# Optimization experiments

Measured on AMD Instinct MI355X. Metric: run time of the kernel, lower is better.

The kernel has to match this reference:

```python
import jax, jax.numpy as jnp
import numpy as np

NUM_LOOP = 10


def gru_cell(x, h, W_ih, W_hh, b_ih, b_hh):
    # torch.nn.GRUCell math. x, h: [N, H]; W_ih, W_hh: [3H, H]; b: [3H]
    gi = x @ W_ih.T + b_ih
    gh = h @ W_hh.T + b_hh
    i_r, i_z, i_n = jnp.split(gi, 3, axis=-1)
    h_r, h_z, h_n = jnp.split(gh, 3, axis=-1)
    r = jax.nn.sigmoid(i_r + h_r)
    z = jax.nn.sigmoid(i_z + h_z)
    n = jnp.tanh(i_n + r * h_n)
    return (1.0 - z) * n + z * h


def setup_inputs() -> dict:
    key = jax.random.key(0)
    ks = jax.random.split(key, 16)
    B, S, L, H, V = 16, 128, 128, 128, 50000
    input_var = jax.random.randint(ks[0], (B, S, L), 0, V, dtype=jnp.int32)
    adjacency = (jax.random.uniform(ks[1], (B, S, L, L)) < 0.05).astype(jnp.float32)
    u = lambda k, shp, a: jax.random.uniform(k, shp, minval=-a, maxval=a, dtype=jnp.float32)
    emb = jax.random.normal(ks[2], (V, H), dtype=jnp.float32) * 0.1
    gnn_w = u(ks[3], (H, H), 0.08)
    gnn_b = u(ks[4], (H,), 0.08)
    W_ih = u(ks[5], (3 * H, H), 0.08)
    W_hh = u(ks[6], (3 * H, H), 0.08)
    b_ih = u(ks[7], (3 * H,), 0.08)
    b_hh = u(ks[8], (3 * H,), 0.08)
    mW1 = u(ks[9], (H, H), 0.08)
    mb1 = u(ks[10], (H,), 0.08)
    mW2 = u(ks[11], (H, H), 0.08)
    mb2 = u(ks[12], (H,), 0.08)
    mW3 = u(ks[13], (1, H), 0.08)
    mb3 = u(ks[14], (1,), 0.08)
    return dict(input_var=input_var, adjacency=adjacency, emb=emb, gnn_w=gnn_w,
                gnn_b=gnn_b, W_ih=W_ih, W_hh=W_hh, b_ih=b_ih, b_hh=b_hh,
                mW1=mW1, mb1=mb1, mW2=mW2, mb2=mb2, mW3=mW3, mb3=mb3)


def reference(input_var, adjacency, emb, gnn_w, gnn_b, W_ih, W_hh, b_ih, b_hh,
              mW1, mb1, mW2, mb2, mW3, mb3):
    B, S, L = input_var.shape
    H = emb.shape[1]
    node_feature = emb[input_var]  # [B, S, L, H]

    def body(i, nf):
        tmp = nf @ gnn_w + gnn_b                      # [B,S,L,H] linear transform
        agg = jnp.matmul(adjacency, tmp)              # [B,S,L,L] @ [B,S,L,H]
        h = gru_cell(agg.reshape(-1, H), nf.reshape(-1, H), W_ih, W_hh, b_ih, b_hh)
        return h.reshape(B, S, L, H)

    node_feature = jax.lax.fori_loop(0, NUM_LOOP, body, node_feature)
    x = node_feature.reshape(B, S * L, H)
    # mention_predictor: 3-layer MLP with tanh after every layer (incl. last)
    h1 = jnp.tanh(x @ mW1.T + mb1)
    h2 = jnp.tanh(h1 @ mW2.T + mb2)
    mention_score = jnp.tanh(h2 @ mW3.T + mb3)        # [B, S*L, 1]
    return mention_score.reshape(B, S * L)
```

## Files before the change

kernel.cpp:

```cpp
#include <hip/hip_runtime.h>
#include <stdint.h>

typedef __bf16 bf16x8 __attribute__((ext_vector_type(8)));
typedef float  f32x4  __attribute__((ext_vector_type(4)));
typedef unsigned short ushortx4 __attribute__((ext_vector_type(4)));

#define LDS_NFROW 0
#define LDS_NFT   32768
#define LDS_P     65536
#define LDS_SAT   98304
#define LDS_RSA   131072
#define LDS_GB2   131584
#define LDS_BIH   133120
#define LDS_BHH   134656
#define LDS_MB1   136192
#define LDS_MB2   136704
#define LDS_TOTAL 137216

#define WS_GW2T   0
#define WS_WHH    98304
#define WS_MW1    196608
#define WS_MW2    229376
#define WS_GB2    262144

__device__ __forceinline__ unsigned short f2bf(float f){
  union{float f; uint32_t u;} v; v.f = f;
  return (unsigned short)((v.u + 0x7FFFu + ((v.u>>16)&1u)) >> 16);
}
__device__ __forceinline__ float bf2f(unsigned short h){
  union{uint32_t u; float f;} v; v.u = ((uint32_t)h)<<16; return v.f;
}
__device__ __forceinline__ float fast_sigmoid(float x){
  float t = __builtin_amdgcn_exp2f(-1.442695041f*x);
  return __builtin_amdgcn_rcpf(1.0f + t);
}
__device__ __forceinline__ float fast_tanh(float x){
  float t = __builtin_amdgcn_exp2f(-2.885390082f*x);
  return 2.0f*__builtin_amdgcn_rcpf(1.0f + t) - 1.0f;
}
__device__ __forceinline__ uint32_t sw(uint32_t row, uint32_t col){
  return row*256u + ((((col>>3) ^ (row&7)) << 4) | ((col&7)<<1));
}

extern "C" __global__ __launch_bounds__(128) void gnn_prep(
    const float* __restrict__ Wih, const float* __restrict__ Whh,
    const float* __restrict__ gnnw, const float* __restrict__ gnnb,
    const float* __restrict__ mW1, const float* __restrict__ mW2,
    unsigned short* __restrict__ gw2t, unsigned short* __restrict__ whhb,
    unsigned short* __restrict__ mw1b, unsigned short* __restrict__ mw2b,
    float* __restrict__ gb2)
{
  __shared__ float wg[128];
  const int b = blockIdx.x, t = threadIdx.x;
  if (b < 384){
    wg[t] = Wih[b*128 + t];
    __syncthreads();
    float acc = 0.f;
    for (int h=0; h<128; ++h) acc += wg[h] * gnnw[t*128 + h];
    gw2t[b*128 + t] = f2bf(acc);
    if (t == 0){
      float a2 = 0.f;
      for (int h=0; h<128; ++h) a2 += wg[h] * gnnb[h];
      gb2[b] = a2;
    }
  } else if (b < 416){
    int base = (b-384)*1536;
    for (int i=t; i<1536; i+=128) whhb[base+i] = f2bf(Whh[base+i]);
  } else if (b < 432){
    int base = (b-416)*1024;
    for (int i=t; i<1024; i+=128) mw1b[base+i] = f2bf(mW1[base+i]);
  } else if (b < 448){
    int base = (b-432)*1024;
    for (int i=t; i<1024; i+=128) mw2b[base+i] = f2bf(mW2[base+i]);
  }
}

extern "C" __global__ __launch_bounds__(512) void gnn_main(
    const int* __restrict__ iv, const float* __restrict__ adj,
    const float* __restrict__ emb,
    const float* __restrict__ bih, const float* __restrict__ bhh,
    const float* __restrict__ mb1, const float* __restrict__ mb2,
    const float* __restrict__ mW3, const float* __restrict__ mb3,
    const __bf16* __restrict__ gw2t, const __bf16* __restrict__ whhb,
    const __bf16* __restrict__ mw1b, const __bf16* __restrict__ mw2b,
    const float* __restrict__ gb2, float* __restrict__ out)
{
  extern __shared__ char lds[];
  const int bs   = blockIdx.x;
  const int tid  = threadIdx.x;
  const int w    = tid >> 6;
  const int lane = tid & 63;
  const int n16  = lane & 15;
  const int q    = lane >> 4;
  const f32x4 zf4 = {0.f, 0.f, 0.f, 0.f};

  if (tid < 384){
    *(float*)(lds + LDS_GB2 + tid*4) = gb2[tid];
    *(float*)(lds + LDS_BIH + tid*4) = bih[tid];
    *(float*)(lds + LDS_BHH + tid*4) = bhh[tid];
  }
  if (tid >= 384){
    int t = tid - 384;
    *(float*)(lds + LDS_MB1 + t*4) = mb1[t];
    *(float*)(lds + LDS_MB2 + t*4) = mb2[t];
  }

  {
    const int l  = tid >> 2;
    const int hc = (tid & 3) * 32;
    const int row = iv[bs*128 + l];
    const float* src = emb + (size_t)row*128 + hc;
    #pragma unroll
    for (int c=0; c<4; ++c){
      float4 f0 = *(const float4*)(src + c*8);
      float4 f1 = *(const float4*)(src + c*8 + 4);
      union{ bf16x8 v; unsigned short s8[8]; } u;
      u.s8[0]=f2bf(f0.x); u.s8[1]=f2bf(f0.y); u.s8[2]=f2bf(f0.z); u.s8[3]=f2bf(f0.w);
      u.s8[4]=f2bf(f1.x); u.s8[5]=f2bf(f1.y); u.s8[6]=f2bf(f1.z); u.s8[7]=f2bf(f1.w);
      *(bf16x8*)(lds + LDS_NFROW + sw(l, hc + c*8)) = u.v;
      #pragma unroll
      for (int j=0; j<8; ++j)
        *(unsigned short*)(lds + LDS_NFT + sw(hc + c*8 + j, l)) = u.s8[j];
    }
  }

  {
    const float* abase = adj + (size_t)bs * 16384;
    #pragma unroll
    for (int k=0; k<4; ++k){
      int s   = k*512 + tid;
      int sl  = s & 63;
      int chk = s >> 6;
      int ltg = chk >> 2, ks = chk & 3;
      int al  = ltg*16 + (sl & 15);
      int ak  = ks*32 + (sl >> 4) * 8;
      const float* p = abase + al*128 + ak;
      float4 f0 = *(const float4*)(p);
      float4 f1 = *(const float4*)(p + 4);
      union{ bf16x8 v; unsigned short s8[8]; } u;
      u.s8[0]=f2bf(f0.x); u.s8[1]=f2bf(f0.y); u.s8[2]=f2bf(f0.z); u.s8[3]=f2bf(f0.w);
      u.s8[4]=f2bf(f1.x); u.s8[5]=f2bf(f1.y); u.s8[6]=f2bf(f1.z); u.s8[7]=f2bf(f1.w);
      *(bf16x8*)(lds + LDS_SAT + s*16) = u.v;
    }
    int l = tid >> 2, p4 = tid & 3;
    const float* p = abase + l*128 + p4*32;
    float ssum = 0.f;
    #pragma unroll
    for (int c=0; c<8; ++c){
      float4 f = *(const float4*)(p + c*4);
      ssum += f.x + f.y + f.z + f.w;
    }
    ssum += __shfl_xor(ssum, 1);
    ssum += __shfl_xor(ssum, 2);
    if (p4 == 0) *(float*)(lds + LDS_RSA + l*4) = ssum;
  }
  __syncthreads();

  const int wr = w & 1, wc = w >> 1;
  const int t0 = wr*64, l0 = wc*32;
  const int h0 = w*16;

  const __bf16* gAr = gw2t + (size_t)(h0       + n16) * 128;
  const __bf16* gAz = gw2t + (size_t)(h0 + 128 + n16) * 128;
  const __bf16* gAn = gw2t + (size_t)(h0 + 256 + n16) * 128;
  const __bf16* hAr = whhb + (size_t)(h0       + n16) * 128;
  const __bf16* hAz = whhb + (size_t)(h0 + 128 + n16) * 128;
  const __bf16* hAn = whhb + (size_t)(h0 + 256 + n16) * 128;

  for (int it=0; it<10; ++it){
    f32x4 accA[4][2];
    #pragma unroll
    for (int a=0; a<4; ++a){ accA[a][0] = zf4; accA[a][1] = zf4; }
    for (int ks=0; ks<4; ++ks){
      bf16x8 af[4];
      #pragma unroll
      for (int tt=0; tt<4; ++tt)
        af[tt] = *(const bf16x8*)(lds + LDS_NFT + sw(t0 + tt*16 + n16, ks*32 + q*8));
      #pragma unroll
      for (int lb=0; lb<2; ++lb){
        int chunk = (wc*2 + lb)*4 + ks;
        bf16x8 bfb = *(const bf16x8*)(lds + LDS_SAT + (chunk*64 + lane)*16);
        #pragma unroll
        for (int tt=0; tt<4; ++tt)
          accA[tt][lb] = __builtin_amdgcn_mfma_f32_16x16x32_bf16(af[tt], bfb, accA[tt][lb], 0,0,0);
      }
    }
    #pragma unroll
    for (int tt=0; tt<4; ++tt){
      #pragma unroll
      for (int lb=0; lb<2; ++lb){
        int l  = l0 + lb*16 + n16;
        int tb = t0 + tt*16 + q*4;
        ushortx4 o4;
        #pragma unroll
        for (int r=0; r<4; ++r) o4[r] = f2bf(accA[tt][lb][r]);
        *(ushortx4*)(lds + LDS_P + sw(l, tb)) = o4;
      }
    }
    __syncthreads();

    f32x4 aR[8], aZ[8], aGN[8], aHN[8];
    #pragma unroll
    for (int i=0; i<8; ++i){ aR[i]=zf4; aZ[i]=zf4; aGN[i]=zf4; aHN[i]=zf4; }
    for (int ks=0; ks<4; ++ks){
      int koff = ks*32 + q*8;
      bf16x8 f_gr = *(const bf16x8*)(gAr + koff);
      bf16x8 f_gz = *(const bf16x8*)(gAz + koff);
      bf16x8 f_gn = *(const bf16x8*)(gAn + koff);
      bf16x8 f_hr = *(const bf16x8*)(hAr + koff);
      bf16x8 f_hz = *(const bf16x8*)(hAz + koff);
      bf16x8 f_hn = *(const bf16x8*)(hAn + koff);
      #pragma unroll
      for (int lt=0; lt<8; ++lt){
        int l = lt*16 + n16;
        bf16x8 bp = *(const bf16x8*)(lds + LDS_P     + sw(l, koff));
        bf16x8 bh = *(const bf16x8*)(lds + LDS_NFROW + sw(l, koff));
        aR[lt]  = __builtin_amdgcn_mfma_f32_16x16x32_bf16(f_gr, bp, aR[lt], 0,0,0);
        aR[lt]  = __builtin_amdgcn_mfma_f32_16x16x32_bf16(f_hr, bh, aR[lt], 0,0,0);
        aZ[lt]  = __builtin_amdgcn_mfma_f32_16x16x32_bf16(f_gz, bp, aZ[lt], 0,0,0);
        aZ[lt]  = __builtin_amdgcn_mfma_f32_16x16x32_bf16(f_hz, bh, aZ[lt], 0,0,0);
        aGN[lt] = __builtin_amdgcn_mfma_f32_16x16x32_bf16(f_gn, bp, aGN[lt], 0,0,0);
        aHN[lt] = __builtin_amdgcn_mfma_f32_16x16x32_bf16(f_hn, bh, aHN[lt], 0,0,0);
      }
    }
    __syncthreads();

    float c_gr[4], c_gz[4], c_gn[4], c_br[4], c_bz[4], c_bin[4], c_bhn[4];
    #pragma unroll
    for (int r=0; r<4; ++r){
      int h = h0 + q*4 + r;
      c_gr[r]  = *(const float*)(lds + LDS_GB2 + h*4);
      c_gz[r]  = *(const float*)(lds + LDS_GB2 + (128+h)*4);
      c_gn[r]  = *(const float*)(lds + LDS_GB2 + (256+h)*4);
      c_br[r]  = *(const float*)(lds + LDS_BIH + h*4)       + *(const float*)(lds + LDS_BHH + h*4);
      c_bz[r]  = *(const float*)(lds + LDS_BIH + (128+h)*4) + *(const float*)(lds + LDS_BHH + (128+h)*4);
      c_bin[r] = *(const float*)(lds + LDS_BIH + (256+h)*4);
      c_bhn[r] = *(const float*)(lds + LDS_BHH + (256+h)*4);
    }
    #pragma unroll
    for (int lt=0; lt<8; ++lt){
      int l = lt*16 + n16;
      float rs = *(const float*)(lds + LDS_RSA + l*4);
      uint32_t a_nf = sw(l, h0 + q*4);
      ushortx4 old4 = *(const ushortx4*)(lds + LDS_NFROW + a_nf);
      ushortx4 new4;
      #pragma unroll
      for (int r=0; r<4; ++r){
        float xr = aR[lt][r] + rs*c_gr[r] + c_br[r];
        float xz = aZ[lt][r] + rs*c_gz[r] + c_bz[r];
        float rg = fast_sigmoid(xr);
        float zg = fast_sigmoid(xz);
        float xn = (aGN[lt][r] + rs*c_gn[r] + c_bin[r]) + rg*(aHN[lt][r] + c_bhn[r]);
        float ng = fast_tanh(xn);
        float hv = bf2f(old4[r]);
        new4[r] = f2bf(ng + zg*(hv - ng));
      }
      *(ushortx4*)(lds + LDS_NFROW + a_nf) = new4;
      #pragma unroll
      for (int r=0; r<4; ++r)
        *(unsigned short*)(lds + LDS_NFT + sw(h0 + q*4 + r, l)) = new4[r];
    }
    __syncthreads();
  }

  {
    f32x4 acc[4][2];
    #pragma unroll
    for (int a=0; a<4; ++a){ acc[a][0] = zf4; acc[a][1] = zf4; }
    for (int ks=0; ks<4; ++ks){
      int koff = ks*32 + q*8;
      bf16x8 af[4];
      #pragma unroll
      for (int tt=0; tt<4; ++tt)
        af[tt] = *(const bf16x8*)(mw1b + (size_t)(t0 + tt*16 + n16)*128 + koff);
      #pragma unroll
      for (int lb=0; lb<2; ++lb){
        int l = l0 + lb*16 + n16;
        bf16x8 bb = *(const bf16x8*)(lds + LDS_NFROW + sw(l, koff));
        #pragma unroll
        for (int tt=0; tt<4; ++tt)
          acc[tt][lb] = __builtin_amdgcn_mfma_f32_16x16x32_bf16(af[tt], bb, acc[tt][lb], 0,0,0);
      }
    }
    #pragma unroll
    for (int tt=0; tt<4; ++tt){
      #pragma unroll
      for (int lb=0; lb<2; ++lb){
        int l  = l0 + lb*16 + n16;
        int ob = t0 + tt*16 + q*4;
        ushortx4 o4;
        #pragma unroll
        for (int r=0; r<4; ++r){
          float bsv = *(const float*)(lds + LDS_MB1 + (ob + r)*4);
          o4[r] = f2bf(fast_tanh(acc[tt][lb][r] + bsv));
        }
        *(ushortx4*)(lds + LDS_P + sw(l, ob)) = o4;
      }
    }
  }
  __syncthreads();

  {
    f32x4 acc[4][2];
    #pragma unroll
    for (int a=0; a<4; ++a){ acc[a][0] = zf4; acc[a][1] = zf4; }
    for (int ks=0; ks<4; ++ks){
      int koff = ks*32 + q*8;
      bf16x8 af[4];
      #pragma unroll
      for (int tt=0; tt<4; ++tt)
        af[tt] = *(const bf16x8*)(mw2b + (size_t)(t0 + tt*16 + n16)*128 + koff);
      #pragma unroll
      for (int lb=0; lb<2; ++lb){
        int l = l0 + lb*16 + n16;
        bf16x8 bb = *(const bf16x8*)(lds + LDS_P + sw(l, koff));
        #pragma unroll
        for (int tt=0; tt<4; ++tt)
          acc[tt][lb] = __builtin_amdgcn_mfma_f32_16x16x32_bf16(af[tt], bb, acc[tt][lb], 0,0,0);
      }
    }
    #pragma unroll
    for (int tt=0; tt<4; ++tt){
      #pragma unroll
      for (int lb=0; lb<2; ++lb){
        int l  = l0 + lb*16 + n16;
        int ob = t0 + tt*16 + q*4;
        ushortx4 o4;
        #pragma unroll
        for (int r=0; r<4; ++r){
          float bsv = *(const float*)(lds + LDS_MB2 + (ob + r)*4);
          o4[r] = f2bf(fast_tanh(acc[tt][lb][r] + bsv));
        }
        *(ushortx4*)(lds + LDS_NFT + sw(l, ob)) = o4;
      }
    }
  }
  __syncthreads();

  {
    int l = tid >> 2, p4 = tid & 3;
    float dot = 0.f;
    #pragma unroll
    for (int c=0; c<4; ++c){
      int o = p4*32 + c*8;
      union{ bf16x8 v; unsigned short s8[8]; } u;
      u.v = *(const bf16x8*)(lds + LDS_NFT + sw(l, o));
      float4 w0 = *(const float4*)(mW3 + o);
      float4 w1 = *(const float4*)(mW3 + o + 4);
      dot += bf2f(u.s8[0])*w0.x + bf2f(u.s8[1])*w0.y + bf2f(u.s8[2])*w0.z + bf2f(u.s8[3])*w0.w
           + bf2f(u.s8[4])*w1.x + bf2f(u.s8[5])*w1.y + bf2f(u.s8[6])*w1.z + bf2f(u.s8[7])*w1.w;
    }
    dot += __shfl_xor(dot, 1);
    dot += __shfl_xor(dot, 2);
    if (p4 == 0) out[bs*128 + l] = fast_tanh(dot + mb3[0]);
  }
}

extern "C" void kernel_launch(void* const* d_in, const int* in_sizes, int n_in,
                              void* d_out, int out_size, void* d_ws, size_t ws_size,
                              hipStream_t stream)
{
  const int*   iv   = (const int*)  d_in[0];
  const float* adj  = (const float*)d_in[1];
  const float* emb  = (const float*)d_in[2];
  const float* gnnw = (const float*)d_in[3];
  const float* gnnb = (const float*)d_in[4];
  const float* Wih  = (const float*)d_in[5];
  const float* Whh  = (const float*)d_in[6];
  const float* bihp = (const float*)d_in[7];
  const float* bhhp = (const float*)d_in[8];
  const float* mW1  = (const float*)d_in[9];
  const float* mb1  = (const float*)d_in[10];
  const float* mW2  = (const float*)d_in[11];
  const float* mb2  = (const float*)d_in[12];
  const float* mW3  = (const float*)d_in[13];
  const float* mb3  = (const float*)d_in[14];
  float* out = (float*)d_out;

  char* ws = (char*)d_ws;
  unsigned short* gw2t_w = (unsigned short*)(ws + WS_GW2T);
  unsigned short* whhb_w = (unsigned short*)(ws + WS_WHH);
  unsigned short* mw1b_w = (unsigned short*)(ws + WS_MW1);
  unsigned short* mw2b_w = (unsigned short*)(ws + WS_MW2);
  float*          gb2_w  = (float*)(ws + WS_GB2);

  hipFuncSetAttribute((const void*)gnn_main,
                      hipFuncAttributeMaxDynamicSharedMemorySize, LDS_TOTAL);

  gnn_prep<<<448, 128, 0, stream>>>(Wih, Whh, gnnw, gnnb, mW1, mW2,
                                    gw2t_w, whhb_w, mw1b_w, mw2b_w, gb2_w);

  int nbs = in_sizes[0] / 128;
  gnn_main<<<nbs, 512, LDS_TOTAL, stream>>>(
      iv, adj, emb, bihp, bhhp, mb1, mb2, mW3, mb3,
      (const __bf16*)gw2t_w, (const __bf16*)whhb_w,
      (const __bf16*)mw1b_w, (const __bf16*)mw2b_w, gb2_w, out);
}
```

Before: 2.244 ms.

## Double block to 1024 threads and stream adjacency from global each iteration

Doubles the workgroup to 16 waves and re-splits every GEMM stage across them: each wave now owns 16 hidden rows by 64 columns in the GNN loop and 32x32 tiles in the MLP. The bf16 adjacency copy in LDS is removed, and adjacency is reloaded from global (fp32, converted each iteration) inside the aggregation loop. This cuts LDS use and register pressure per wave so more waves can hide latency. The biases are packed into one per-row structure and the swizzle gets an extra XOR term to reduce bank conflicts. The cost is ten re-reads of the adjacency tile from global or cache plus repeated conversion work.

```diff
diff --git a/kernel.cpp b/kernel.cpp
--- a/kernel.cpp
+++ b/kernel.cpp
@@ -8,14 +8,11 @@
 #define LDS_NFROW 0
 #define LDS_NFT   32768
 #define LDS_P     65536
-#define LDS_SAT   98304
-#define LDS_RSA   131072
-#define LDS_GB2   131584
-#define LDS_BIH   133120
-#define LDS_BHH   134656
-#define LDS_MB1   136192
-#define LDS_MB2   136704
-#define LDS_TOTAL 137216
+#define LDS_RSA   98304
+#define LDS_CB    98816
+#define LDS_MB1   102912
+#define LDS_MB2   103424
+#define LDS_TOTAL 103936
 
 #define WS_GW2T   0
 #define WS_WHH    98304
@@ -39,7 +36,7 @@
   return 2.0f*__builtin_amdgcn_rcpf(1.0f + t) - 1.0f;
 }
 __device__ __forceinline__ uint32_t sw(uint32_t row, uint32_t col){
-  return row*256u + ((((col>>3) ^ (row&7)) << 4) | ((col&7)<<1));
+  return row*256u + ((((col>>3) ^ (row&7) ^ ((row>>3)&3)) << 4) | ((col&7)<<1));
 }
 
 extern "C" __global__ __launch_bounds__(128) void gnn_prep(
@@ -75,7 +72,7 @@
   }
 }
 
-extern "C" __global__ __launch_bounds__(512) void gnn_main(
+extern "C" __global__ __launch_bounds__(1024) void gnn_main(
     const int* __restrict__ iv, const float* __restrict__ adj,
     const float* __restrict__ emb,
     const float* __restrict__ bih, const float* __restrict__ bhh,
@@ -94,163 +91,141 @@
   const int q    = lane >> 4;
   const f32x4 zf4 = {0.f, 0.f, 0.f, 0.f};
 
-  if (tid < 384){
-    *(float*)(lds + LDS_GB2 + tid*4) = gb2[tid];
-    *(float*)(lds + LDS_BIH + tid*4) = bih[tid];
-    *(float*)(lds + LDS_BHH + tid*4) = bhh[tid];
-  }
-  if (tid >= 384){
-    int t = tid - 384;
+  const int hw = w >> 1, lc = w & 1;
+  const int t0  = hw*16;
+  const int h0  = t0;
+  const int lG0 = lc*64;
+  const int wr = w >> 2, wc = w & 3;
+  const int tm0 = wr*32, lm0 = wc*32;
+
+  if (tid < 128){
+    int h = tid;
+    float* cb = (float*)(lds + LDS_CB + h*32);
+    cb[0] = gb2[h]; cb[1] = gb2[128+h]; cb[2] = gb2[256+h];
+    cb[3] = bih[h] + bhh[h];
+    cb[4] = bih[128+h] + bhh[128+h];
+    cb[5] = bih[256+h];
+    cb[6] = bhh[256+h];
+    cb[7] = 0.f;
+  } else if (tid < 256){
+    int t = tid - 128;
     *(float*)(lds + LDS_MB1 + t*4) = mb1[t];
     *(float*)(lds + LDS_MB2 + t*4) = mb2[t];
   }
-
   {
-    const int l  = tid >> 2;
-    const int hc = (tid & 3) * 32;
+    const int l   = tid >> 3;
+    const int hc8 = (tid & 7) * 16;
     const int row = iv[bs*128 + l];
-    const float* src = emb + (size_t)row*128 + hc;
-    #pragma unroll
-    for (int c=0; c<4; ++c){
+    const float* src = emb + (size_t)row*128 + hc8;
+    #pragma unroll
+    for (int c=0; c<2; ++c){
       float4 f0 = *(const float4*)(src + c*8);
       float4 f1 = *(const float4*)(src + c*8 + 4);
       union{ bf16x8 v; unsigned short s8[8]; } u;
       u.s8[0]=f2bf(f0.x); u.s8[1]=f2bf(f0.y); u.s8[2]=f2bf(f0.z); u.s8[3]=f2bf(f0.w);
       u.s8[4]=f2bf(f1.x); u.s8[5]=f2bf(f1.y); u.s8[6]=f2bf(f1.z); u.s8[7]=f2bf(f1.w);
-      *(bf16x8*)(lds + LDS_NFROW + sw(l, hc + c*8)) = u.v;
+      *(bf16x8*)(lds + LDS_NFROW + sw(l, hc8 + c*8)) = u.v;
       #pragma unroll
       for (int j=0; j<8; ++j)
-        *(unsigned short*)(lds + LDS_NFT + sw(hc + c*8 + j, l)) = u.s8[j];
-    }
-  }
-
-  {
-    const float* abase = adj + (size_t)bs * 16384;
-    #pragma unroll
-    for (int k=0; k<4; ++k){
-      int s   = k*512 + tid;
-      int sl  = s & 63;
-      int chk = s >> 6;
-      int ltg = chk >> 2, ks = chk & 3;
-      int al  = ltg*16 + (sl & 15);
-      int ak  = ks*32 + (sl >> 4) * 8;
-      const float* p = abase + al*128 + ak;
-      float4 f0 = *(const float4*)(p);
-      float4 f1 = *(const float4*)(p + 4);
-      union{ bf16x8 v; unsigned short s8[8]; } u;
-      u.s8[0]=f2bf(f0.x); u.s8[1]=f2bf(f0.y); u.s8[2]=f2bf(f0.z); u.s8[3]=f2bf(f0.w);
-      u.s8[4]=f2bf(f1.x); u.s8[5]=f2bf(f1.y); u.s8[6]=f2bf(f1.z); u.s8[7]=f2bf(f1.w);
-      *(bf16x8*)(lds + LDS_SAT + s*16) = u.v;
-    }
-    int l = tid >> 2, p4 = tid & 3;
-    const float* p = abase + l*128 + p4*32;
-    float ssum = 0.f;
-    #pragma unroll
-    for (int c=0; c<8; ++c){
-      float4 f = *(const float4*)(p + c*4);
-      ssum += f.x + f.y + f.z + f.w;
-    }
-    ssum += __shfl_xor(ssum, 1);
-    ssum += __shfl_xor(ssum, 2);
-    if (p4 == 0) *(float*)(lds + LDS_RSA + l*4) = ssum;
+        *(unsigned short*)(lds + LDS_NFT + sw(hc8 + c*8 + j, l)) = u.s8[j];
+    }
+    const float* ap = adj + (size_t)bs*16384 + l*128 + hc8;
+    float s = 0.f;
+    #pragma unroll
+    for (int c=0; c<4; ++c){
+      float4 f = *(const float4*)(ap + c*4);
+      s += f.x + f.y + f.z + f.w;
+    }
+    s += __shfl_xor(s, 1);
+    s += __shfl_xor(s, 2);
+    s += __shfl_xor(s, 4);
+    if ((tid & 7) == 0) *(float*)(lds + LDS_RSA + l*4) = s;
   }
   __syncthreads();
 
-  const int wr = w & 1, wc = w >> 1;
-  const int t0 = wr*64, l0 = wc*32;
-  const int h0 = w*16;
-
-  const __bf16* gAr = gw2t + (size_t)(h0       + n16) * 128;
-  const __bf16* gAz = gw2t + (size_t)(h0 + 128 + n16) * 128;
-  const __bf16* gAn = gw2t + (size_t)(h0 + 256 + n16) * 128;
-  const __bf16* hAr = whhb + (size_t)(h0       + n16) * 128;
-  const __bf16* hAz = whhb + (size_t)(h0 + 128 + n16) * 128;
-  const __bf16* hAn = whhb + (size_t)(h0 + 256 + n16) * 128;
+  const __bf16* gR = gw2t + (size_t)(h0       + n16) * 128;
+  const __bf16* gZ = gw2t + (size_t)(h0 + 128 + n16) * 128;
+  const __bf16* gN = gw2t + (size_t)(h0 + 256 + n16) * 128;
+  const __bf16* hR = whhb + (size_t)(h0       + n16) * 128;
+  const __bf16* hZ = whhb + (size_t)(h0 + 128 + n16) * 128;
+  const __bf16* hN = whhb + (size_t)(h0 + 256 + n16) * 128;
+  const float*  abase = adj + (size_t)bs * 16384;
 
   for (int it=0; it<10; ++it){
-    f32x4 accA[4][2];
-    #pragma unroll
-    for (int a=0; a<4; ++a){ accA[a][0] = zf4; accA[a][1] = zf4; }
+    f32x4 accA[4];
+    #pragma unroll
+    for (int j=0; j<4; ++j) accA[j] = zf4;
     for (int ks=0; ks<4; ++ks){
-      bf16x8 af[4];
-      #pragma unroll
-      for (int tt=0; tt<4; ++tt)
-        af[tt] = *(const bf16x8*)(lds + LDS_NFT + sw(t0 + tt*16 + n16, ks*32 + q*8));
-      #pragma unroll
-      for (int lb=0; lb<2; ++lb){
-        int chunk = (wc*2 + lb)*4 + ks;
-        bf16x8 bfb = *(const bf16x8*)(lds + LDS_SAT + (chunk*64 + lane)*16);
-        #pragma unroll
-        for (int tt=0; tt<4; ++tt)
-          accA[tt][lb] = __builtin_amdgcn_mfma_f32_16x16x32_bf16(af[tt], bfb, accA[tt][lb], 0,0,0);
-      }
-    }
-    #pragma unroll
-    for (int tt=0; tt<4; ++tt){
-      #pragma unroll
-      for (int lb=0; lb<2; ++lb){
-        int l  = l0 + lb*16 + n16;
-        int tb = t0 + tt*16 + q*4;
-        ushortx4 o4;
-        #pragma unroll
-        for (int r=0; r<4; ++r) o4[r] = f2bf(accA[tt][lb][r]);
-        *(ushortx4*)(lds + LDS_P + sw(l, tb)) = o4;
-      }
-    }
-    __syncthreads();
-
-    f32x4 aR[8], aZ[8], aGN[8], aHN[8];
-    #pragma unroll
-    for (int i=0; i<8; ++i){ aR[i]=zf4; aZ[i]=zf4; aGN[i]=zf4; aHN[i]=zf4; }
+      bf16x8 af = *(const bf16x8*)(lds + LDS_NFT + sw(t0 + n16, ks*32 + q*8));
+      #pragma unroll
+      for (int j=0; j<4; ++j){
+        int al = lG0 + j*16 + n16;
+        const float* ap = abase + al*128 + ks*32 + q*8;
+        float4 a0 = *(const float4*)(ap);
+        float4 a1 = *(const float4*)(ap + 4);
+        union{ bf16x8 v; unsigned short s8[8]; } u;
+        u.s8[0]=f2bf(a0.x); u.s8[1]=f2bf(a0.y); u.s8[2]=f2bf(a0.z); u.s8[3]=f2bf(a0.w);
+        u.s8[4]=f2bf(a1.x); u.s8[5]=f2bf(a1.y); u.s8[6]=f2bf(a1.z); u.s8[7]=f2bf(a1.w);
+        accA[j] = __builtin_amdgcn_mfma_f32_16x16x32_bf16(af, u.v, accA[j], 0,0,0);
+      }
+    }
+    #pragma unroll
+    for (int j=0; j<4; ++j){
+      int l = lG0 + j*16 + n16;
+      ushortx4 o4;
+      #pragma unroll
+      for (int r=0; r<4; ++r) o4[r] = f2bf(accA[j][r]);
+      *(ushortx4*)(lds + LDS_P + sw(l, t0 + q*4)) = o4;
+    }
+    __syncthreads();
+
+    f32x4 aR[4], aZ[4], aGN[4], aHN[4];
+    #pragma unroll
+    for (int i=0; i<4; ++i){ aR[i]=zf4; aZ[i]=zf4; aGN[i]=zf4; aHN[i]=zf4; }
     for (int ks=0; ks<4; ++ks){
       int koff = ks*32 + q*8;
-      bf16x8 f_gr = *(const bf16x8*)(gAr + koff);
-      bf16x8 f_gz = *(const bf16x8*)(gAz + koff);
-      bf16x8 f_gn = *(const bf16x8*)(gAn + koff);
-      bf16x8 f_hr = *(const bf16x8*)(hAr + koff);
-      bf16x8 f_hz = *(const bf16x8*)(hAz + koff);
-      bf16x8 f_hn = *(const bf16x8*)(hAn + koff);
-      #pragma unroll
-      for (int lt=0; lt<8; ++lt){
-        int l = lt*16 + n16;
+      bf16x8 f_gr = *(const bf16x8*)(gR + koff);
+      bf16x8 f_gz = *(const bf16x8*)(gZ + koff);
+      bf16x8 f_gn = *(const bf16x8*)(gN + koff);
+      bf16x8 f_hr = *(const bf16x8*)(hR + koff);
+      bf16x8 f_hz = *(const bf16x8*)(hZ + koff);
+      bf16x8 f_hn = *(const bf16x8*)(hN + koff);
+      #pragma unroll
+      for (int lt=0; lt<4; ++lt){
+        int l = lG0 + lt*16 + n16;
         bf16x8 bp = *(const bf16x8*)(lds + LDS_P     + sw(l, koff));
         bf16x8 bh = *(const bf16x8*)(lds + LDS_NFROW + sw(l, koff));
         aR[lt]  = __builtin_amdgcn_mfma_f32_16x16x32_bf16(f_gr, bp, aR[lt], 0,0,0);
+        aZ[lt]  = __builtin_amdgcn_mfma_f32_16x16x32_bf16(f_gz, bp, aZ[lt], 0,0,0);
+        aGN[lt] = __builtin_amdgcn_mfma_f32_16x16x32_bf16(f_gn, bp, aGN[lt], 0,0,0);
         aR[lt]  = __builtin_amdgcn_mfma_f32_16x16x32_bf16(f_hr, bh, aR[lt], 0,0,0);
-        aZ[lt]  = __builtin_amdgcn_mfma_f32_16x16x32_bf16(f_gz, bp, aZ[lt], 0,0,0);
         aZ[lt]  = __builtin_amdgcn_mfma_f32_16x16x32_bf16(f_hz, bh, aZ[lt], 0,0,0);
-        aGN[lt] = __builtin_amdgcn_mfma_f32_16x16x32_bf16(f_gn, bp, aGN[lt], 0,0,0);
         aHN[lt] = __builtin_amdgcn_mfma_f32_16x16x32_bf16(f_hn, bh, aHN[lt], 0,0,0);
       }
     }
     __syncthreads();
 
-    float c_gr[4], c_gz[4], c_gn[4], c_br[4], c_bz[4], c_bin[4], c_bhn[4];
+    f32x4 cbA[4], cbB[4];
     #pragma unroll
     for (int r=0; r<4; ++r){
       int h = h0 + q*4 + r;
-      c_gr[r]  = *(const float*)(lds + LDS_GB2 + h*4);
-      c_gz[r]  = *(const float*)(lds + LDS_GB2 + (128+h)*4);
-      c_gn[r]  = *(const float*)(lds + LDS_GB2 + (256+h)*4);
-      c_br[r]  = *(const float*)(lds + LDS_BIH + h*4)       + *(const float*)(lds + LDS_BHH + h*4);
-      c_bz[r]  = *(const float*)(lds + LDS_BIH + (128+h)*4) + *(const float*)(lds + LDS_BHH + (128+h)*4);
-      c_bin[r] = *(const float*)(lds + LDS_BIH + (256+h)*4);
-      c_bhn[r] = *(const float*)(lds + LDS_BHH + (256+h)*4);
-    }
-    #pragma unroll
-    for (int lt=0; lt<8; ++lt){
-      int l = lt*16 + n16;
+      cbA[r] = *(const f32x4*)(lds + LDS_CB + h*32);
+      cbB[r] = *(const f32x4*)(lds + LDS_CB + h*32 + 16);
+    }
+    #pragma unroll
+    for (int lt=0; lt<4; ++lt){
+      int l = lG0 + lt*16 + n16;
       float rs = *(const float*)(lds + LDS_RSA + l*4);
       uint32_t a_nf = sw(l, h0 + q*4);
       ushortx4 old4 = *(const ushortx4*)(lds + LDS_NFROW + a_nf);
       ushortx4 new4;
       #pragma unroll
       for (int r=0; r<4; ++r){
-        float xr = aR[lt][r] + rs*c_gr[r] + c_br[r];
-        float xz = aZ[lt][r] + rs*c_gz[r] + c_bz[r];
+        float xr = aR[lt][r] + rs*cbA[r][0] + cbA[r][3];
+        float xz = aZ[lt][r] + rs*cbA[r][1] + cbB[r][0];
         float rg = fast_sigmoid(xr);
         float zg = fast_sigmoid(xz);
-        float xn = (aGN[lt][r] + rs*c_gn[r] + c_bin[r]) + rg*(aHN[lt][r] + c_bhn[r]);
+        float xn = (aGN[lt][r] + rs*cbA[r][2] + cbB[r][1]) + rg*(aHN[lt][r] + cbB[r][2]);
         float ng = fast_tanh(xn);
         float hv = bf2f(old4[r]);
         new4[r] = f2bf(ng + zg*(hv - ng));
@@ -264,30 +239,31 @@
   }
 
   {
-    f32x4 acc[4][2];
-    #pragma unroll
-    for (int a=0; a<4; ++a){ acc[a][0] = zf4; acc[a][1] = zf4; }
+    f32x4 acc[2][2];
+    #pragma unroll
+    for (int a=0; a<2; ++a){ acc[a][0] = zf4; acc[a][1] = zf4; }
     for (int ks=0; ks<4; ++ks){
       int koff = ks*32 + q*8;
-      bf16x8 af[4];
-      #pragma unroll
-      for (int tt=0; tt<4; ++tt)
-        af[tt] = *(const bf16x8*)(mw1b + (size_t)(t0 + tt*16 + n16)*128 + koff);
+      bf16x8 af[2];
+      #pragma unroll
+      for (int tt=0; tt<2; ++tt)
+        af[tt] = *(const bf16x8*)(mw1b + (size_t)(tm0 + tt*16 + n16)*128 + koff);
       #pragma unroll
       for (int lb=0; lb<2; ++lb){
-        int l = l0 + lb*16 + n16;
+        int l = lm0 + lb*16 + n16;
         bf16x8 bb = *(const bf16x8*)(lds + LDS_NFROW + sw(l, koff));
         #pragma unroll
-        for (int tt=0; tt<4; ++tt)
+        for (int tt=0; tt<2; ++tt)
           acc[tt][lb] = __builtin_amdgcn_mfma_f32_16x16x32_bf16(af[tt], bb, acc[tt][lb], 0,0,0);
       }
     }
-    #pragma unroll
-    for (int tt=0; tt<4; ++tt){
+    __syncthreads();
+    #pragma unroll
+    for (int tt=0; tt<2; ++tt){
       #pragma unroll
       for (int lb=0; lb<2; ++lb){
-        int l  = l0 + lb*16 + n16;
-        int ob = t0 + tt*16 + q*4;
+        int l  = lm0 + lb*16 + n16;
+        int ob = tm0 + tt*16 + q*4;
         ushortx4 o4;
         #pragma unroll
         for (int r=0; r<4; ++r){
@@ -301,30 +277,30 @@
   __syncthreads();
 
   {
-    f32x4 acc[4][2];
-    #pragma unroll
-    for (int a=0; a<4; ++a){ acc[a][0] = zf4; acc[a][1] = zf4; }
+    f32x4 acc[2][2];
+    #pragma unroll
+    for (int a=0; a<2; ++a){ acc[a][0] = zf4; acc[a][1] = zf4; }
     for (int ks=0; ks<4; ++ks){
       int koff = ks*32 + q*8;
-      bf16x8 af[4];
-      #pragma unroll
-      for (int tt=0; tt<4; ++tt)
-        af[tt] = *(const bf16x8*)(mw2b + (size_t)(t0 + tt*16 + n16)*128 + koff);
+      bf16x8 af[2];
+      #pragma unroll
+      for (int tt=0; tt<2; ++tt)
+        af[tt] = *(const bf16x8*)(mw2b + (size_t)(tm0 + tt*16 + n16)*128 + koff);
       #pragma unroll
       for (int lb=0; lb<2; ++lb){
-        int l = l0 + lb*16 + n16;
+        int l = lm0 + lb*16 + n16;
         bf16x8 bb = *(const bf16x8*)(lds + LDS_P + sw(l, koff));
         #pragma unroll
-        for (int tt=0; tt<4; ++tt)
+        for (int tt=0; tt<2; ++tt)
           acc[tt][lb] = __builtin_amdgcn_mfma_f32_16x16x32_bf16(af[tt], bb, acc[tt][lb], 0,0,0);
       }
     }
     #pragma unroll
-    for (int tt=0; tt<4; ++tt){
+    for (int tt=0; tt<2; ++tt){
       #pragma unroll
       for (int lb=0; lb<2; ++lb){
-        int l  = l0 + lb*16 + n16;
-        int ob = t0 + tt*16 + q*4;
+        int l  = lm0 + lb*16 + n16;
+        int ob = tm0 + tt*16 + q*4;
         ushortx4 o4;
         #pragma unroll
         for (int r=0; r<4; ++r){
@@ -338,11 +314,11 @@
   __syncthreads();
 
   {
-    int l = tid >> 2, p4 = tid & 3;
+    int l = tid >> 3, p8 = tid & 7;
     float dot = 0.f;
     #pragma unroll
-    for (int c=0; c<4; ++c){
-      int o = p4*32 + c*8;
+    for (int c=0; c<2; ++c){
+      int o = p8*16 + c*8;
       union{ bf16x8 v; unsigned short s8[8]; } u;
       u.v = *(const bf16x8*)(lds + LDS_NFT + sw(l, o));
       float4 w0 = *(const float4*)(mW3 + o);
@@ -352,7 +328,8 @@
     }
     dot += __shfl_xor(dot, 1);
     dot += __shfl_xor(dot, 2);
-    if (p4 == 0) out[bs*128 + l] = fast_tanh(dot + mb3[0]);
+    dot += __shfl_xor(dot, 4);
+    if (p8 == 0) out[bs*128 + l] = fast_tanh(dot + mb3[0]);
   }
 }
 
@@ -391,7 +368,7 @@
                                     gw2t_w, whhb_w, mw1b_w, mw2b_w, gb2_w);
 
   int nbs = in_sizes[0] / 128;
-  gnn_main<<<nbs, 512, LDS_TOTAL, stream>>>(
+  gnn_main<<<nbs, 1024, LDS_TOTAL, stream>>>(
       iv, adj, emb, bihp, bhhp, mb1, mb2, mW3, mb3,
       (const __bf16*)gw2t_w, (const __bf16*)whhb_w,
       (const __bf16*)mw1b_w, (const __bf16*)mw2b_w, gb2_w, out);
```

Result: slower. 3.620 ms (+61.3%).
